# Performance work log

Measured on AMD Instinct MI355X. Metric: run time of the kernel, lower is better.

Reference implementation:

```python
import jax, jax.numpy as jnp
import numpy as np
from jax import lax

NH = 4          # num_head
DIM = 512       # attention dim
VDIM = 512      # v_dim
QDIM = 1024     # q_dim
KS = 100        # loc_kernel_size -> conv width 2*KS+1
KN = 100        # loc_kernel_num
TEMP = 0.5      # temperature
BS, TS = 8, 2048


def setup_inputs() -> dict:
    key = jax.random.key(0)
    ks = jax.random.split(key, 12)
    s = 0.05
    return {
        "dec_state": jax.random.normal(ks[0], (BS, QDIM), jnp.float32),
        "enc_feat": jax.random.normal(ks[1], (BS, TS, VDIM), jnp.float32),
        "enc_len": jax.random.randint(ks[2], (BS,), TS // 2, TS + 1).astype(jnp.int32),
        "Wq": jax.random.normal(ks[3], (NH * DIM, QDIM), jnp.float32) * s,
        "bq": jnp.zeros((NH * DIM,), jnp.float32),
        "Wk": jax.random.normal(ks[4], (NH * DIM, VDIM), jnp.float32) * s,
        "bk": jnp.zeros((NH * DIM,), jnp.float32),
        "Wv": jax.random.normal(ks[5], (NH * VDIM, VDIM), jnp.float32) * s,
        "bv": jnp.zeros((NH * VDIM,), jnp.float32),
        "loc_conv_w": jax.random.normal(ks[6], (KN, NH, 2 * KS + 1), jnp.float32) * s,
        "loc_proj_w": jax.random.normal(ks[7], (DIM, KN), jnp.float32) * s,
        "gen_w": jax.random.normal(ks[8], (1, DIM), jnp.float32) * s,
        "gen_b": jnp.zeros((1,), jnp.float32),
        "merge_w": jax.random.normal(ks[9], (VDIM, NH * VDIM), jnp.float32) * s,
        "merge_b": jnp.zeros((VDIM,), jnp.float32),
    }


def reference(dec_state, enc_feat, enc_len, Wq, bq, Wk, bk, Wv, bv,
              loc_conv_w, loc_proj_w, gen_w, gen_b, merge_w, merge_b):
    bs, ts, _ = enc_feat.shape
    # query: [bs, nh, dim]
    query = jnp.tanh(dec_state @ Wq.T + bq).reshape(bs, NH, DIM)
    # key/value: [bs, nh, ts, dim]/[bs, nh, ts, v_dim]
    key = jnp.tanh(enc_feat @ Wk.T + bk).reshape(bs, ts, NH, DIM).transpose(0, 2, 1, 3)
    value = jnp.tanh(enc_feat @ Wv.T + bv).reshape(bs, ts, NH, VDIM).transpose(0, 2, 1, 3)
    # mask & initial (uniform-over-valid) previous attention
    pos = jnp.arange(ts)
    pad_mask = pos[None, :] >= enc_len[:, None]                      # [bs, ts] True = padded
    prev = jnp.where(pad_mask, 0.0, 1.0 / enc_len[:, None].astype(jnp.float32))  # [bs, ts]
    prev_att = jnp.broadcast_to(prev[:, None, :], (bs, NH, ts))      # [bs, nh, ts]
    # location features: Conv1d(nh -> kn, width 2*KS+1, pad KS, no bias)
    conv = lax.conv_general_dilated(prev_att, loc_conv_w, (1,), [(KS, KS)],
                                    dimension_numbers=("NCH", "OIH", "NCH"))  # [bs, kn, ts]
    loc = jnp.tanh(jnp.einsum("bkt,dk->btd", conv, loc_proj_w))      # [bs, ts, dim]
    # additive energy: gen_energy(tanh(k + q + loc))
    e = jnp.tanh(key + query[:, :, None, :] + loc[:, None, :, :])    # [bs, nh, ts, dim]
    energy = jnp.einsum("bhtd,d->bht", e, gen_w[0]) + gen_b[0]
    energy = energy / TEMP
    energy = jnp.where(pad_mask[:, None, :], -jnp.inf, energy)
    attn = jax.nn.softmax(energy, axis=-1)                           # [bs, nh, ts]
    ctx = jnp.einsum("bht,bhtv->bhv", attn, value).reshape(bs, NH * VDIM)
    context = ctx @ merge_w.T + merge_b                              # [bs, v_dim]
    return attn, context
```

## Files before the change

kernel.cpp:

```cpp
#include <hip/hip_runtime.h>
#include <math.h>

#define NH 4
#define DIM 512
#define VDIM 512
#define QDIM 1024
#define KS 100
#define KN 100
#define TEMPERATURE 0.5f
#define BS 8
#define TS 2048
#define NHD (NH * DIM)

#define WS_QUERY   0
#define WS_QTAB    16384
#define WS_ENERGYP 119808
#define WS_CTX     381952
#define WS_P       398336
#define WS_F32_END 418536

typedef __bf16 bf16x8 __attribute__((ext_vector_type(8)));
typedef __bf16 bf16x4 __attribute__((ext_vector_type(4)));
typedef float  f32x4  __attribute__((ext_vector_type(4)));

#define AS1(p) ((const __attribute__((address_space(1))) void*)(p))
#define AS3(p) ((__attribute__((address_space(3))) void*)(p))

__device__ __forceinline__ float fast_tanh(float x) {
    float e = __expf(2.0f * x);
    return 1.0f - __fdividef(2.0f, e + 1.0f);
}

#define NE4 (BS * TS * VDIM / 4)
#define NW4 (NHD * VDIM / 4)
#define NCVT ((NE4 + 2 * NW4) / 256)
#define NQ2  (NHD / 4)
__global__ void k_pre(const float* __restrict__ enc, const float* __restrict__ Wk,
                      const float* __restrict__ Wv, __bf16* __restrict__ enc_bf,
                      __bf16* __restrict__ wk_bf, __bf16* __restrict__ wv_bf,
                      const float* __restrict__ dec, const float* __restrict__ Wq,
                      const float* __restrict__ bq, float* __restrict__ query,
                      const float* __restrict__ convw, float* __restrict__ P) {
    const int bx = blockIdx.x;
    if (bx < NCVT) {
        int i = bx * blockDim.x + threadIdx.x;
        const float* src; __bf16* dst; int k;
        if (i < NE4)            { src = enc; dst = enc_bf; k = i; }
        else if (i < NE4 + NW4) { src = Wk;  dst = wk_bf;  k = i - NE4; }
        else                    { src = Wv;  dst = wv_bf;  k = i - NE4 - NW4; }
        float4 v = ((const float4*)src)[k];
        bf16x4 o;
        o[0] = (__bf16)v.x; o[1] = (__bf16)v.y; o[2] = (__bf16)v.z; o[3] = (__bf16)v.w;
        ((bf16x4*)dst)[k] = o;
    } else if (bx < NCVT + NQ2) {
        int o = (bx - NCVT) * 4 + (threadIdx.x >> 6);
        int lane = threadIdx.x & 63;
        const float* wr = Wq + (size_t)o * QDIM;
        float s[BS];
        #pragma unroll
        for (int b = 0; b < BS; ++b) s[b] = 0.f;
        #pragma unroll
        for (int i = 0; i < QDIM / 64; ++i) {
            float wv = wr[lane + 64 * i];
            #pragma unroll
            for (int b = 0; b < BS; ++b)
                s[b] = fmaf(wv, dec[b * QDIM + lane + 64 * i], s[b]);
        }
        #pragma unroll
        for (int off = 32; off > 0; off >>= 1)
            #pragma unroll
            for (int b = 0; b < BS; ++b) s[b] += __shfl_down(s[b], off);
        if (lane == 0) {
            float bias = bq[o];
            #pragma unroll
            for (int b = 0; b < BS; ++b) query[b * NHD + o] = tanhf(s[b] + bias);
        }
    } else {
        __shared__ float cs[KN * (2 * KS + 1)];
        int tid = threadIdx.x;
        for (int i = tid; i < KN * (2 * KS + 1); i += 256) {
            int k = i / (2 * KS + 1);
            int dt = i - k * (2 * KS + 1);
            const float* wr = convw + k * (NH * (2 * KS + 1)) + dt;
            cs[i] = wr[0] + wr[201] + wr[402] + wr[603];
        }
        __syncthreads();
        if (tid < KN) {
            float acc = 0.f;
            P[tid] = 0.f;
            const float* c = cs + tid * (2 * KS + 1);
            for (int dt = 0; dt < 2 * KS + 1; ++dt) {
                acc += c[dt];
                P[(dt + 1) * KN + tid] = acc;
            }
        }
    }
}

__global__ void k_qtab(const float* __restrict__ P, const float* __restrict__ projw,
                       float* __restrict__ Qtab, float* __restrict__ ctx) {
    int tid = threadIdx.x;
    if (blockIdx.x >= 2 * KS + 2) {
        int z = (blockIdx.x - (2 * KS + 2)) * 512 + tid;
        ((float4*)ctx)[z] = make_float4(0.f, 0.f, 0.f, 0.f);
        return;
    }
    int j = blockIdx.x;
    __shared__ float Pc[KN];
    if (tid < KN) Pc[tid] = P[j * KN + tid];
    __syncthreads();
    const float* pr = projw + tid * KN;
    float s = 0.f;
    #pragma unroll 4
    for (int k = 0; k < KN; ++k) s = fmaf(pr[k], Pc[k], s);
    Qtab[j * DIM + tid] = s;
}

#define GEMM1(Bptr)                                                               \
    const int bid = blockIdx.x;                                                    \
    const int b   = bid >> 8;                                                      \
    const int t0  = ((bid >> 4) & 15) << 7;                                        \
    const int n0  = ((((bid >> 3) & 1) << 3) | (bid & 7)) << 7;                    \
    const int len = enc_len[b];                                                    \
    if (t0 >= len) return;                                                         \
    const int tid = threadIdx.x;                                                   \
    const int w = tid >> 6, lane = tid & 63;                                       \
    const int wy = w >> 2, wx = w & 3;                                             \
    const int col = lane & 15, quad = lane >> 4;                                   \
    __shared__ __bf16 Ash[2 * 4096];                                               \
    __shared__ __bf16 Bsh[2 * 4096];                                               \
    f32x4 acc[4][2];                                                               \
    _Pragma("unroll")                                                              \
    for (int i = 0; i < 4; ++i)                                                    \
        _Pragma("unroll")                                                          \
        for (int j = 0; j < 2; ++j) acc[i][j] = (f32x4)0.f;                        \
    const __bf16* Abase = enc_bf + ((size_t)b * TS + t0) * VDIM;                   \
    const int sm = tid >> 2;                                                       \
    const int sj = (tid & 3) ^ (sm & 3) ^ ((sm >> 2) & 3);                         \
    const __bf16* gpA = Abase + (size_t)sm * VDIM + sj * 8;                        \
    const __bf16* gpB = (Bptr) + ((size_t)n0 + sm) * VDIM + sj * 8;                \
    const int cfr = quad ^ (col & 3) ^ ((col >> 2) & 3);                           \
    const char* pA = (const char*)Ash + (((wy * 64 + col) * 4 + cfr) << 4);        \
    const char* pB = (const char*)Bsh + (((wx * 32 + col) * 4 + cfr) << 4);        \
    __builtin_amdgcn_global_load_lds(AS1(gpA), AS3(Ash + w * 512), 16, 0, 0);      \
    __builtin_amdgcn_global_load_lds(AS1(gpB), AS3(Bsh + w * 512), 16, 0, 0);      \
    gpA += 32; gpB += 32;                                                          \
    for (int kk = 0; kk < 16; ++kk) {                                              \
        __syncthreads();                                                           \
        if (kk < 15) {                                                             \
            int nb_ = ((kk + 1) & 1) * 4096;                                       \
            __builtin_amdgcn_global_load_lds(AS1(gpA), AS3(Ash + nb_ + w * 512), 16, 0, 0); \
            __builtin_amdgcn_global_load_lds(AS1(gpB), AS3(Bsh + nb_ + w * 512), 16, 0, 0); \
            gpA += 32; gpB += 32;                                                  \
        }                                                                          \
        const int bo = (kk & 1) * 8192;                                            \
        bf16x8 af[4], bfr[2];                                                      \
        _Pragma("unroll")                                                          \
        for (int i = 0; i < 4; ++i) af[i] = *(const bf16x8*)(pA + bo + i * 1024);  \
        _Pragma("unroll")                                                          \
        for (int j = 0; j < 2; ++j) bfr[j] = *(const bf16x8*)(pB + bo + j * 1024); \
        _Pragma("unroll")                                                          \
        for (int i = 0; i < 4; ++i)                                                \
            _Pragma("unroll")                                                      \
            for (int j = 0; j < 2; ++j)                                            \
                acc[i][j] = __builtin_amdgcn_mfma_f32_16x16x32_bf16(               \
                    af[i], bfr[j], acc[i][j], 0, 0, 0);                            \
    }                                                                              \
    __syncthreads();

__global__ __launch_bounds__(512, 4) void k_energy(
    const __bf16* __restrict__ enc_bf, const __bf16* __restrict__ wk_bf,
    const float* __restrict__ bk, const float* __restrict__ gen_w,
    const int* __restrict__ enc_len, const float* __restrict__ query,
    const float* __restrict__ Qtab, float* __restrict__ energyP) {
    GEMM1(wk_bf)

    const int h = n0 >> 9;
    const float inv_len = 1.0f / (float)len;
    float qv[2], gw[2], bkv[2], lI[2];
    int dj[2];
    #pragma unroll
    for (int j = 0; j < 2; ++j) {
        int n = n0 + wx * 32 + j * 16 + col;
        dj[j] = n & (DIM - 1);
        qv[j] = query[b * NHD + n];
        gw[j] = gen_w[dj[j]];
        bkv[j] = bk[n];
        lI[j] = fast_tanh((Qtab[(2 * KS + 1) * DIM + dj[j]] - Qtab[dj[j]]) * inv_len);
    }
    float* red = (float*)Ash;
    #pragma unroll
    for (int i = 0; i < 4; ++i) {
        #pragma unroll
        for (int r = 0; r < 4; ++r) {
            int tl = wy * 64 + i * 16 + quad * 4 + r;
            int t = t0 + tl;
            float l[2];
            if (t >= KS && t < len - KS) {
                #pragma unroll
                for (int j = 0; j < 2; ++j) l[j] = lI[j];
            } else {
                int lo = KS - t; if (lo < 0) lo = 0;
                int hi = KS - t + len - 1; if (hi > 2 * KS) hi = 2 * KS;
                bool has = (hi >= lo);
                #pragma unroll
                for (int j = 0; j < 2; ++j) {
                    float cv = has
                        ? (Qtab[(hi + 1) * DIM + dj[j]] - Qtab[lo * DIM + dj[j]]) * inv_len
                        : 0.f;
                    l[j] = fast_tanh(cv);
                }
            }
            float s = 0.f;
            #pragma unroll
            for (int j = 0; j < 2; ++j) {
                float key = fast_tanh(acc[i][j][r] + bkv[j]);
                float e = fast_tanh(key + qv[j] + l[j]);
                s = fmaf(e, gw[j], s);
            }
            s += __shfl_xor(s, 1); s += __shfl_xor(s, 2);
            s += __shfl_xor(s, 4); s += __shfl_xor(s, 8);
            if (col == 0) red[tl * 4 + wx] = s;
        }
    }
    __syncthreads();
    if (tid < 128) {
        float s = red[tid * 4] + red[tid * 4 + 1] + red[tid * 4 + 2] + red[tid * 4 + 3];
        energyP[(size_t)((n0 >> 7) & 3) * 65536 + (size_t)(b * NH + h) * TS + t0 + tid] = s;
    }
}

__global__ __launch_bounds__(512, 4) void k_ctxg(
    const __bf16* __restrict__ enc_bf, const __bf16* __restrict__ wv_bf,
    const float* __restrict__ bv, const float* __restrict__ attn,
    const int* __restrict__ enc_len, float* __restrict__ ctx) {
    GEMM1(wv_bf)

    const int h = n0 >> 9;
    float att[4][4];
    #pragma unroll
    for (int i = 0; i < 4; ++i)
        #pragma unroll
        for (int r = 0; r < 4; ++r)
            att[i][r] = attn[(size_t)(b * NH + h) * TS + t0 + wy * 64 + i * 16 + quad * 4 + r];
    float* red = (float*)Ash;
    #pragma unroll
    for (int j = 0; j < 2; ++j) {
        int nl = wx * 32 + j * 16 + col;
        float bvn = bv[n0 + nl];
        float s = 0.f;
        #pragma unroll
        for (int i = 0; i < 4; ++i)
            #pragma unroll
            for (int r = 0; r < 4; ++r)
                s = fmaf(att[i][r], fast_tanh(acc[i][j][r] + bvn), s);
        s += __shfl_xor(s, 16); s += __shfl_xor(s, 32);
        if (quad == 0) red[nl * 2 + wy] = s;
    }
    __syncthreads();
    if (tid < 128) {
        float s = red[tid * 2] + red[tid * 2 + 1];
        atomicAdd(&ctx[(size_t)b * NHD + n0 + tid], s);
    }
}

__global__ void k_softmax(const float* __restrict__ energyP, const int* __restrict__ enc_len,
                          const float* __restrict__ gen_b, float* __restrict__ attn) {
    int bh = blockIdx.x;
    int b = bh >> 2;
    int len = enc_len[b];
    int tid = threadIdx.x;
    int w = tid >> 6, lane = tid & 63;
    const float gb = gen_b[0];
    const float* e0 = energyP + (size_t)bh * TS;
    float ev[4];
    float mx = -INFINITY;
    #pragma unroll
    for (int i = 0; i < 4; ++i) {
        int t = i * 512 + tid;
        float e = -INFINITY;
        if (t < len) {
            float s = e0[t] + e0[65536 + t] + e0[131072 + t] + e0[196608 + t];
            e = (s + gb) * (1.0f / TEMPERATURE);
        }
        ev[i] = e;
        mx = fmaxf(mx, e);
    }
    __shared__ float sred[8], ssum[8];
    #pragma unroll
    for (int off = 32; off > 0; off >>= 1) mx = fmaxf(mx, __shfl_xor(mx, off));
    if (lane == 0) sred[w] = mx;
    __syncthreads();
    #pragma unroll
    for (int k = 0; k < 8; ++k) mx = fmaxf(mx, sred[k]);
    float ls = 0.f;
    #pragma unroll
    for (int i = 0; i < 4; ++i) {
        float ex = __expf(ev[i] - mx);
        ev[i] = ex;
        ls += ex;
    }
    #pragma unroll
    for (int off = 32; off > 0; off >>= 1) ls += __shfl_xor(ls, off);
    if (lane == 0) ssum[w] = ls;
    __syncthreads();
    float tot = 0.f;
    #pragma unroll
    for (int k = 0; k < 8; ++k) tot += ssum[k];
    float inv = 1.0f / tot;
    #pragma unroll
    for (int i = 0; i < 4; ++i)
        attn[(size_t)bh * TS + i * 512 + tid] = ev[i] * inv;
}

__global__ void k_merge(const float* __restrict__ ctx, const float* __restrict__ mw,
                        const float* __restrict__ mb, float* __restrict__ out) {
    int o = blockIdx.x * 4 + (threadIdx.x >> 6);
    int lane = threadIdx.x & 63;
    const float* wr = mw + (size_t)o * NHD;
    float s[BS];
    #pragma unroll
    for (int b = 0; b < BS; ++b) s[b] = 0.f;
    #pragma unroll
    for (int i = 0; i < NHD / 64; ++i) {
        float wv = wr[lane + 64 * i];
        #pragma unroll
        for (int b = 0; b < BS; ++b)
            s[b] = fmaf(wv, ctx[b * NHD + lane + 64 * i], s[b]);
    }
    #pragma unroll
    for (int off = 32; off > 0; off >>= 1)
        #pragma unroll
        for (int b = 0; b < BS; ++b) s[b] += __shfl_down(s[b], off);
    if (lane == 0) {
        float bias = mb[o];
        #pragma unroll
        for (int b = 0; b < BS; ++b) out[b * VDIM + o] = s[b] + bias;
    }
}

extern "C" void kernel_launch(void* const* d_in, const int* in_sizes, int n_in,
                              void* d_out, int out_size, void* d_ws, size_t ws_size,
                              hipStream_t stream) {
    const float* dec     = (const float*)d_in[0];
    const float* enc     = (const float*)d_in[1];
    const int*   enc_len = (const int*)d_in[2];
    const float* Wq      = (const float*)d_in[3];
    const float* bq      = (const float*)d_in[4];
    const float* Wk      = (const float*)d_in[5];
    const float* bk      = (const float*)d_in[6];
    const float* Wv      = (const float*)d_in[7];
    const float* bv      = (const float*)d_in[8];
    const float* convw   = (const float*)d_in[9];
    const float* projw   = (const float*)d_in[10];
    const float* gen_w   = (const float*)d_in[11];
    const float* gen_b   = (const float*)d_in[12];
    const float* merge_w = (const float*)d_in[13];
    const float* merge_b = (const float*)d_in[14];

    float* out    = (float*)d_out;
    float* ws     = (float*)d_ws;
    float* query  = ws + WS_QUERY;
    float* Qtab   = ws + WS_QTAB;
    float* energyP= ws + WS_ENERGYP;
    float* ctx    = ws + WS_CTX;
    float* Pws    = ws + WS_P;
    __bf16* enc_bf = (__bf16*)((char*)d_ws + (size_t)WS_F32_END * 4);
    __bf16* wk_bf  = enc_bf + (size_t)BS * TS * VDIM;
    __bf16* wv_bf  = wk_bf + (size_t)NHD * VDIM;

    k_pre<<<dim3(NCVT + NQ2 + 1), dim3(256), 0, stream>>>(
        enc, Wk, Wv, enc_bf, wk_bf, wv_bf, dec, Wq, bq, query, convw, Pws);
    k_qtab<<<dim3(2 * KS + 2 + 8), dim3(512), 0, stream>>>(Pws, projw, Qtab, ctx);
    k_energy<<<dim3(2048), dim3(512), 0, stream>>>(
        enc_bf, wk_bf, bk, gen_w, enc_len, query, Qtab, energyP);
    k_softmax<<<dim3(BS * NH), dim3(512), 0, stream>>>(energyP, enc_len, gen_b, out);
    k_ctxg<<<dim3(2048), dim3(512), 0, stream>>>(
        enc_bf, wv_bf, bv, out, enc_len, ctx);
    k_merge<<<dim3(VDIM / 4), dim3(256), 0, stream>>>(ctx, merge_w, merge_b, out + 65536);
}
```

Before: 309.2 us.

## Fuse key and value GEMMs into one kernel, materialize fp16 values

The key-projection energy GEMM and the value-projection GEMM now run in one kernel that shares each loaded enc tile, so enc_bf is read once instead of twice and one large launch is removed. The tanh'd values are written to global memory as fp16, and a new lightweight kernel does the attention-weighted reduction after softmax. The K loop also moves from double to triple buffering with explicit waitcnt and barrier instructions. In exchange there is an extra 64MB fp16 write and read, more shared memory per block, extra accumulator registers, and fp16 rounding of the values.

```diff
diff --git a/kernel.cpp b/kernel.cpp
--- a/kernel.cpp
+++ b/kernel.cpp
@@ -21,6 +21,7 @@
 
 typedef __bf16 bf16x8 __attribute__((ext_vector_type(8)));
 typedef __bf16 bf16x4 __attribute__((ext_vector_type(4)));
+typedef _Float16 f16x8 __attribute__((ext_vector_type(8)));
 typedef float  f32x4  __attribute__((ext_vector_type(4)));
 
 #define AS1(p) ((const __attribute__((address_space(1))) void*)(p))
@@ -116,68 +117,83 @@
     Qtab[j * DIM + tid] = s;
 }
 
-#define GEMM1(Bptr)                                                               \
-    const int bid = blockIdx.x;                                                    \
-    const int b   = bid >> 8;                                                      \
-    const int t0  = ((bid >> 4) & 15) << 7;                                        \
-    const int n0  = ((((bid >> 3) & 1) << 3) | (bid & 7)) << 7;                    \
-    const int len = enc_len[b];                                                    \
-    if (t0 >= len) return;                                                         \
-    const int tid = threadIdx.x;                                                   \
-    const int w = tid >> 6, lane = tid & 63;                                       \
-    const int wy = w >> 2, wx = w & 3;                                             \
-    const int col = lane & 15, quad = lane >> 4;                                   \
-    __shared__ __bf16 Ash[2 * 4096];                                               \
-    __shared__ __bf16 Bsh[2 * 4096];                                               \
-    f32x4 acc[4][2];                                                               \
-    _Pragma("unroll")                                                              \
-    for (int i = 0; i < 4; ++i)                                                    \
-        _Pragma("unroll")                                                          \
-        for (int j = 0; j < 2; ++j) acc[i][j] = (f32x4)0.f;                        \
-    const __bf16* Abase = enc_bf + ((size_t)b * TS + t0) * VDIM;                   \
-    const int sm = tid >> 2;                                                       \
-    const int sj = (tid & 3) ^ (sm & 3) ^ ((sm >> 2) & 3);                         \
-    const __bf16* gpA = Abase + (size_t)sm * VDIM + sj * 8;                        \
-    const __bf16* gpB = (Bptr) + ((size_t)n0 + sm) * VDIM + sj * 8;                \
-    const int cfr = quad ^ (col & 3) ^ ((col >> 2) & 3);                           \
-    const char* pA = (const char*)Ash + (((wy * 64 + col) * 4 + cfr) << 4);        \
-    const char* pB = (const char*)Bsh + (((wx * 32 + col) * 4 + cfr) << 4);        \
-    __builtin_amdgcn_global_load_lds(AS1(gpA), AS3(Ash + w * 512), 16, 0, 0);      \
-    __builtin_amdgcn_global_load_lds(AS1(gpB), AS3(Bsh + w * 512), 16, 0, 0);      \
-    gpA += 32; gpB += 32;                                                          \
-    for (int kk = 0; kk < 16; ++kk) {                                              \
-        __syncthreads();                                                           \
-        if (kk < 15) {                                                             \
-            int nb_ = ((kk + 1) & 1) * 4096;                                       \
-            __builtin_amdgcn_global_load_lds(AS1(gpA), AS3(Ash + nb_ + w * 512), 16, 0, 0); \
-            __builtin_amdgcn_global_load_lds(AS1(gpB), AS3(Bsh + nb_ + w * 512), 16, 0, 0); \
-            gpA += 32; gpB += 32;                                                  \
-        }                                                                          \
-        const int bo = (kk & 1) * 8192;                                            \
-        bf16x8 af[4], bfr[2];                                                      \
-        _Pragma("unroll")                                                          \
-        for (int i = 0; i < 4; ++i) af[i] = *(const bf16x8*)(pA + bo + i * 1024);  \
-        _Pragma("unroll")                                                          \
-        for (int j = 0; j < 2; ++j) bfr[j] = *(const bf16x8*)(pB + bo + j * 1024); \
-        _Pragma("unroll")                                                          \
-        for (int i = 0; i < 4; ++i)                                                \
-            _Pragma("unroll")                                                      \
-            for (int j = 0; j < 2; ++j)                                            \
-                acc[i][j] = __builtin_amdgcn_mfma_f32_16x16x32_bf16(               \
-                    af[i], bfr[j], acc[i][j], 0, 0, 0);                            \
-    }                                                                              \
-    __syncthreads();
-
-__global__ __launch_bounds__(512, 4) void k_energy(
+__global__ __launch_bounds__(512, 4) void k_fused(
     const __bf16* __restrict__ enc_bf, const __bf16* __restrict__ wk_bf,
-    const float* __restrict__ bk, const float* __restrict__ gen_w,
+    const __bf16* __restrict__ wv_bf, const float* __restrict__ bk,
+    const float* __restrict__ bv, const float* __restrict__ gen_w,
     const int* __restrict__ enc_len, const float* __restrict__ query,
-    const float* __restrict__ Qtab, float* __restrict__ energyP) {
-    GEMM1(wk_bf)
+    const float* __restrict__ Qtab, float* __restrict__ energyP,
+    _Float16* __restrict__ val) {
+    const int bid = blockIdx.x;
+    const int b   = bid >> 8;
+    const int t0  = ((bid >> 4) & 15) << 7;
+    const int n0  = ((((bid >> 3) & 1) << 3) | (bid & 7)) << 7;
+    const int len = enc_len[b];
+    if (t0 >= len) return;
+    const int tid = threadIdx.x;
+    const int w = tid >> 6, lane = tid & 63;
+    const int wy = w >> 2, wx = w & 3;
+    const int col = lane & 15, quad = lane >> 4;
+    __shared__ __bf16 smem[3 * 12288];
+    f32x4 accE[4][2], accV[4][2];
+    #pragma unroll
+    for (int i = 0; i < 4; ++i)
+        #pragma unroll
+        for (int j = 0; j < 2; ++j) { accE[i][j] = (f32x4)0.f; accV[i][j] = (f32x4)0.f; }
+    const int sm = tid >> 2;
+    const int sj = (tid & 3) ^ (sm & 3) ^ ((sm >> 2) & 3);
+    const __bf16* gpA  = enc_bf + ((size_t)b * TS + t0) * VDIM + (size_t)sm * VDIM + sj * 8;
+    const __bf16* gpBk = wk_bf + ((size_t)n0 + sm) * VDIM + sj * 8;
+    const __bf16* gpBv = wv_bf + ((size_t)n0 + sm) * VDIM + sj * 8;
+    const int cfr = quad ^ (col & 3) ^ ((col >> 2) & 3);
+    const char* pbase = (const char*)smem;
+    const int offA = (((wy * 64 + col) * 4 + cfr) << 4);
+    const int offB = (((wx * 32 + col) * 4 + cfr) << 4);
+    #define STG(sbe)                                                               \
+        __builtin_amdgcn_global_load_lds(AS1(gpA),  AS3(smem + (sbe) + w * 512), 16, 0, 0);        \
+        __builtin_amdgcn_global_load_lds(AS1(gpBk), AS3(smem + (sbe) + 4096 + w * 512), 16, 0, 0); \
+        __builtin_amdgcn_global_load_lds(AS1(gpBv), AS3(smem + (sbe) + 8192 + w * 512), 16, 0, 0); \
+        gpA += 32; gpBk += 32; gpBv += 32;
+    STG(0)
+    STG(12288)
+    #pragma unroll
+    for (int kk = 0; kk < 16; ++kk) {
+        if (kk < 15)
+            asm volatile("s_waitcnt vmcnt(3) lgkmcnt(0)\n\ts_barrier" ::: "memory");
+        else
+            asm volatile("s_waitcnt vmcnt(0) lgkmcnt(0)\n\ts_barrier" ::: "memory");
+        if (kk < 14) {
+            const int sbe = ((kk + 2) % 3) * 12288;
+            STG(sbe)
+        }
+        const int bo = (kk % 3) * 24576;
+        bf16x8 af[4], bfr[2];
+        #pragma unroll
+        for (int i = 0; i < 4; ++i) af[i] = *(const bf16x8*)(pbase + bo + offA + i * 1024);
+        #pragma unroll
+        for (int j = 0; j < 2; ++j) bfr[j] = *(const bf16x8*)(pbase + bo + 8192 + offB + j * 1024);
+        #pragma unroll
+        for (int i = 0; i < 4; ++i)
+            #pragma unroll
+            for (int j = 0; j < 2; ++j)
+                accE[i][j] = __builtin_amdgcn_mfma_f32_16x16x32_bf16(af[i], bfr[j], accE[i][j], 0, 0, 0);
+        #pragma unroll
+        for (int j = 0; j < 2; ++j) bfr[j] = *(const bf16x8*)(pbase + bo + 16384 + offB + j * 1024);
+        #pragma unroll
+        for (int i = 0; i < 4; ++i)
+            #pragma unroll
+            for (int j = 0; j < 2; ++j)
+                accV[i][j] = __builtin_amdgcn_mfma_f32_16x16x32_bf16(af[i], bfr[j], accV[i][j], 0, 0, 0);
+    }
+    #undef STG
+    __syncthreads();
+
+    _Float16* stage = (_Float16*)smem;
+    float* red = (float*)((char*)smem + 32768);
 
     const int h = n0 >> 9;
     const float inv_len = 1.0f / (float)len;
-    float qv[2], gw[2], bkv[2], lI[2];
+    float qv[2], gw[2], bkv[2], bvv[2], lI[2];
     int dj[2];
     #pragma unroll
     for (int j = 0; j < 2; ++j) {
@@ -186,9 +202,9 @@
         qv[j] = query[b * NHD + n];
         gw[j] = gen_w[dj[j]];
         bkv[j] = bk[n];
+        bvv[j] = bv[n];
         lI[j] = fast_tanh((Qtab[(2 * KS + 1) * DIM + dj[j]] - Qtab[dj[j]]) * inv_len);
     }
-    float* red = (float*)Ash;
     #pragma unroll
     for (int i = 0; i < 4; ++i) {
         #pragma unroll
@@ -214,7 +230,7 @@
             float s = 0.f;
             #pragma unroll
             for (int j = 0; j < 2; ++j) {
-                float key = fast_tanh(acc[i][j][r] + bkv[j]);
+                float key = fast_tanh(accE[i][j][r] + bkv[j]);
                 float e = fast_tanh(key + qv[j] + l[j]);
                 s = fmaf(e, gw[j], s);
             }
@@ -223,44 +239,28 @@
             if (col == 0) red[tl * 4 + wx] = s;
         }
     }
+    #pragma unroll
+    for (int j = 0; j < 2; ++j) {
+        #pragma unroll
+        for (int i = 0; i < 4; ++i)
+            #pragma unroll
+            for (int r = 0; r < 4; ++r) {
+                int tl = wy * 64 + i * 16 + quad * 4 + r;
+                stage[tl * 128 + wx * 32 + j * 16 + col] =
+                    (_Float16)fast_tanh(accV[i][j][r] + bvv[j]);
+            }
+    }
     __syncthreads();
     if (tid < 128) {
         float s = red[tid * 4] + red[tid * 4 + 1] + red[tid * 4 + 2] + red[tid * 4 + 3];
         energyP[(size_t)((n0 >> 7) & 3) * 65536 + (size_t)(b * NH + h) * TS + t0 + tid] = s;
     }
-}
-
-__global__ __launch_bounds__(512, 4) void k_ctxg(
-    const __bf16* __restrict__ enc_bf, const __bf16* __restrict__ wv_bf,
-    const float* __restrict__ bv, const float* __restrict__ attn,
-    const int* __restrict__ enc_len, float* __restrict__ ctx) {
-    GEMM1(wv_bf)
-
-    const int h = n0 >> 9;
-    float att[4][4];
-    #pragma unroll
-    for (int i = 0; i < 4; ++i)
-        #pragma unroll
-        for (int r = 0; r < 4; ++r)
-            att[i][r] = attn[(size_t)(b * NH + h) * TS + t0 + wy * 64 + i * 16 + quad * 4 + r];
-    float* red = (float*)Ash;
-    #pragma unroll
-    for (int j = 0; j < 2; ++j) {
-        int nl = wx * 32 + j * 16 + col;
-        float bvn = bv[n0 + nl];
-        float s = 0.f;
-        #pragma unroll
-        for (int i = 0; i < 4; ++i)
-            #pragma unroll
-            for (int r = 0; r < 4; ++r)
-                s = fmaf(att[i][r], fast_tanh(acc[i][j][r] + bvn), s);
-        s += __shfl_xor(s, 16); s += __shfl_xor(s, 32);
-        if (quad == 0) red[nl * 2 + wy] = s;
-    }
-    __syncthreads();
-    if (tid < 128) {
-        float s = red[tid * 2] + red[tid * 2 + 1];
-        atomicAdd(&ctx[(size_t)b * NHD + n0 + tid], s);
+    #pragma unroll
+    for (int it = 0; it < 4; ++it) {
+        int idx = it * 512 + tid;
+        int row = idx >> 4, seg = idx & 15;
+        *(float4*)((char*)(val + ((size_t)b * TS + t0 + row) * NHD + n0) + seg * 16) =
+            ((const float4*)stage)[idx];
     }
 }
 
@@ -311,6 +311,44 @@
     #pragma unroll
     for (int i = 0; i < 4; ++i)
         attn[(size_t)bh * TS + i * 512 + tid] = ev[i] * inv;
+}
+
+__global__ __launch_bounds__(256) void k_ctx2(const _Float16* __restrict__ val,
+                                              const float* __restrict__ attn,
+                                              const int* __restrict__ enc_len,
+                                              float* __restrict__ ctx) {
+    const int blk = blockIdx.x;
+    const int b   = blk >> 7;
+    const int nc  = (blk >> 3) & 15;
+    const int tsl = blk & 7;
+    const int len = enc_len[b];
+    const int t0  = tsl * 256;
+    if (t0 >= len) return;
+    const int n0 = nc * 128;
+    const int h  = n0 >> 9;
+    const int tid = threadIdx.x;
+    const int tn = tid & 15, tr = tid >> 4;
+    const float* ar = attn + (size_t)(b * NH + h) * TS;
+    float acc[8];
+    #pragma unroll
+    for (int k = 0; k < 8; ++k) acc[k] = 0.f;
+    int tend = t0 + 256; if (tend > len) tend = len;
+    for (int t = t0 + tr; t < tend; t += 16) {
+        float a = ar[t];
+        f16x8 v = *(const f16x8*)(val + ((size_t)b * TS + t) * NHD + n0 + tn * 8);
+        #pragma unroll
+        for (int k = 0; k < 8; ++k) acc[k] = fmaf(a, (float)v[k], acc[k]);
+    }
+    __shared__ float cred[16][128];
+    #pragma unroll
+    for (int k = 0; k < 8; ++k) cred[tr][tn * 8 + k] = acc[k];
+    __syncthreads();
+    if (tid < 128) {
+        float s = 0.f;
+        #pragma unroll
+        for (int r = 0; r < 16; ++r) s += cred[r][tid];
+        atomicAdd(&ctx[(size_t)b * NHD + n0 + tid], s);
+    }
 }
 
 __global__ void k_merge(const float* __restrict__ ctx, const float* __restrict__ mw,
@@ -368,14 +406,14 @@
     __bf16* enc_bf = (__bf16*)((char*)d_ws + (size_t)WS_F32_END * 4);
     __bf16* wk_bf  = enc_bf + (size_t)BS * TS * VDIM;
     __bf16* wv_bf  = wk_bf + (size_t)NHD * VDIM;
+    _Float16* val  = (_Float16*)(wv_bf + (size_t)NHD * VDIM);
 
     k_pre<<<dim3(NCVT + NQ2 + 1), dim3(256), 0, stream>>>(
         enc, Wk, Wv, enc_bf, wk_bf, wv_bf, dec, Wq, bq, query, convw, Pws);
     k_qtab<<<dim3(2 * KS + 2 + 8), dim3(512), 0, stream>>>(Pws, projw, Qtab, ctx);
-    k_energy<<<dim3(2048), dim3(512), 0, stream>>>(
-        enc_bf, wk_bf, bk, gen_w, enc_len, query, Qtab, energyP);
+    k_fused<<<dim3(2048), dim3(512), 0, stream>>>(
+        enc_bf, wk_bf, wv_bf, bk, bv, gen_w, enc_len, query, Qtab, energyP, val);
     k_softmax<<<dim3(BS * NH), dim3(512), 0, stream>>>(energyP, enc_len, gen_b, out);
-    k_ctxg<<<dim3(2048), dim3(512), 0, stream>>>(
-        enc_bf, wv_bf, bv, out, enc_len, ctx);
+    k_ctx2<<<dim3(BS * 16 * 8), dim3(256), 0, stream>>>(val, out, enc_len, ctx);
     k_merge<<<dim3(VDIM / 4), dim3(256), 0, stream>>>(ctx, merge_w, merge_b, out + 65536);
 }
```

Result: faster. 287.7 us (median of 2 runs) (-6.9%).
